# Kernel tuning notes

Hardware: AMD Instinct MI355X
Metric: run time of the kernel (lower is better)

Reference implementation:

```python
import jax, jax.numpy as jnp
import numpy as np

NUM_HEADS = 16
HEAD_DIM = 128
EMBED = NUM_HEADS * HEAD_DIM  # 2048
BATCH, SEQ = 2, 2048


def setup_inputs() -> dict:
    key = jax.random.key(0)
    k1, k2 = jax.random.split(key)
    x = jax.random.normal(k1, (BATCH, SEQ, EMBED), dtype=jnp.float32)
    W = jax.random.normal(k2, (EMBED, 3 * EMBED), dtype=jnp.float32) * 0.02
    b = jnp.zeros((3 * EMBED,), dtype=jnp.float32)
    return {"x": x, "W": W, "b": b}


def _rotate_half(u):
    u1, u2 = jnp.split(u, 2, axis=-1)
    return jnp.concatenate([-u2, u1], axis=-1)


def reference(x, W, b):
    B, S, E = x.shape
    H, D = NUM_HEADS, HEAD_DIM
    # Fused QKV projection: [B,S,E] @ [E,3E] -> [B,S,3E]
    qkv = jnp.einsum('bse,ef->bsf', x, W) + b
    qkv = qkv.reshape(B, S, 3, H, D)
    q, k, v = qkv[:, :, 0], qkv[:, :, 1], qkv[:, :, 2]  # each [B,S,H,D]
    # Module's rotary embedding: sin/cos over arange(S*D), shared across heads
    t = jnp.arange(S * D, dtype=jnp.float32).reshape(1, S, 1, D)
    sin, cos = jnp.sin(t), jnp.cos(t)
    q = q * cos + _rotate_half(q) * sin
    k = k * cos + _rotate_half(k) * sin
    # Scaled dot-product attention over sequence, per head
    scale = 1.0 / jnp.sqrt(jnp.float32(D))
    attn = jnp.einsum('bqhd,bkhd->bhqk', q, k) * scale  # [B,H,S,S]
    w = jax.nn.softmax(attn, axis=-1)
    out = jnp.einsum('bhqk,bkhd->bqhd', w, v)  # [B,S,H,D]
    return out
```

## Files before the change

### kernel.cpp

```cpp
#include <hip/hip_runtime.h>
#include <stdint.h>

typedef unsigned short u16;
typedef __attribute__((ext_vector_type(8))) short bf16x8;
typedef __attribute__((ext_vector_type(4))) float f32x4;

#define NUM_B 2
#define SEQ   2048
#define SEQP  2080
#define NH    16
#define HD    128
#define EMB   2048
#define N3    6144
#define MM    4096
#define QT    256
#define WQ    32
#define KT    64
#define NTILE (SEQ / KT)

#define BM 128
#define BN 384
#define BK 64
#define NT_K (EMB / BK)

__device__ __forceinline__ u16 f2bf(float f) {
  union { float f; unsigned u; } c; c.f = f;
  return (u16)((c.u + 0x7FFFu + ((c.u >> 16) & 1u)) >> 16);
}
__device__ __forceinline__ void async16(const void* g, void* l) {
  __builtin_amdgcn_global_load_lds(
      (const __attribute__((address_space(1))) void*)g,
      (__attribute__((address_space(3))) void*)l, 16, 0, 0);
}
__device__ __forceinline__ uint32_t cvtpk_bf16(float lo, float hi) {
  uint32_t r;
  asm("v_cvt_pk_bf16_f32 %0, %1, %2" : "=v"(r) : "v"(lo), "v"(hi));
  return r;
}

#define GBAR()   asm volatile("s_barrier" ::: "memory")

#define CVT_BLKS (MM * EMB / 4 / 256)
#define TRN_BX   (N3 / 32)
__global__ void k_prep(const float* __restrict__ x, u16* __restrict__ xb,
                       float2* __restrict__ tab,
                       const float* __restrict__ W, u16* __restrict__ Wt) {
  __shared__ float t[32][33];
  const int bid = blockIdx.x;
  if (bid < CVT_BLKS) {
    int i = bid * 256 + threadIdx.x;
    const float4 v = ((const float4*)x)[i];
    ushort4 o;
    o.x = f2bf(v.x); o.y = f2bf(v.y); o.z = f2bf(v.z); o.w = f2bf(v.w);
    ((ushort4*)xb)[i] = o;
    if (i < SEQ * HD) {
      double tt = (double)i;
      tab[i] = make_float2((float)cos(tt), (float)sin(tt));
    }
  } else {
    int b2 = bid - CVT_BLKS;
    int n0 = (b2 % TRN_BX) * 32, k0 = (b2 / TRN_BX) * 32;
    int tx = threadIdx.x & 31, ty = threadIdx.x >> 5;
    #pragma unroll
    for (int i = ty; i < 32; i += 8)
      t[i][tx] = W[(size_t)(k0 + i) * N3 + n0 + tx];
    __syncthreads();
    #pragma unroll
    for (int i = ty; i < 32; i += 8)
      Wt[(size_t)(n0 + i) * EMB + k0 + tx] = f2bf(t[tx][i]);
  }
}

__global__ __launch_bounds__(512, 2) void k_gemm_qkv(
    const u16* __restrict__ xb, const u16* __restrict__ wt,
    const float* __restrict__ bias, const float2* __restrict__ tab,
    u16* __restrict__ qb, u16* __restrict__ kb, u16* __restrict__ vbt)
{
  __shared__ __align__(16) u16 lsA[2][BM * BK];
  __shared__ __align__(16) u16 lsB[2][BN * BK];
  const int tid = threadIdx.x;
  const int wave = tid >> 6, lane = tid & 63;
  const int lq = lane & 15, lr = lane >> 4;
  const int wr = wave >> 2, wc = wave & 3;
  const int m0 = blockIdx.y * BM, n0 = blockIdx.x * BN;

  auto stA = [&](int t) {
    const int kt = t * BK;
    #pragma unroll
    for (int ii = 0; ii < 2; ++ii) {
      int s = ii * 512 + tid;
      int row = s >> 3, gq = (s & 7) ^ (row & 7);
      async16(xb + (size_t)(m0 + row) * EMB + kt + gq * 8, &lsA[t & 1][s * 8]);
    }
  };
  auto stB = [&](int t, int u) {
    const int kt = t * BK;
    #pragma unroll
    for (int ii = 0; ii < 2; ++ii) {
      int s = u * 1024 + ii * 512 + tid;
      int row = s >> 3, gq = (s & 7) ^ (row & 7);
      async16(wt + (size_t)(n0 + row) * EMB + kt + gq * 8, &lsB[t & 1][s * 8]);
    }
  };

  f32x4 acc[4][6];
  #pragma unroll
  for (int i = 0; i < 4; ++i)
    #pragma unroll
    for (int j = 0; j < 6; ++j)
      acc[i][j] = f32x4{0.f, 0.f, 0.f, 0.f};

  int rbase[6];
  #pragma unroll
  for (int nf = 0; nf < 6; ++nf) {
    int pg = 3 * wc + (nf >> 1);
    int col = (pg >> 2) * 128 + (pg & 3) * 16 + (nf & 1) * 64 + lq;
    rbase[nf] = col * BK;
  }
  const int aRow0 = (wr * 64 + lq) * BK;
  int qsw[2];
  qsw[0] = ((0 + lr) ^ (lq & 7)) * 8;
  qsw[1] = ((4 + lr) ^ (lq & 7)) * 8;

  stA(0); stB(0, 0); stB(0, 1); stB(0, 2); stB(1, 0); stB(1, 1); stB(1, 2);
  asm volatile("s_waitcnt vmcnt(6)" ::: "memory");
  GBAR();

  for (int ti = 0; ti < NT_K / 2; ++ti) {
    const int t0 = 2 * ti, t1 = t0 + 1;
    const bool nl = (ti < NT_K / 2 - 1);

    #pragma unroll
    for (int hp = 0; hp < 2; ++hp) {
      const u16* Ap = lsA[hp];
      const u16* Bp = lsB[hp];
      bf16x8 bfr[6][2];

      #pragma unroll
      for (int ph = 0; ph < 2; ++ph) {
        if (ph == 0) {
          #pragma unroll
          for (int nf = 0; nf < 6; ++nf)
            #pragma unroll
            for (int kk = 0; kk < 2; ++kk)
              bfr[nf][kk] = *(const bf16x8*)(Bp + rbase[nf] + qsw[kk]);
        }
        bf16x8 af[2][2];
        #pragma unroll
        for (int mfl = 0; mfl < 2; ++mfl)
          #pragma unroll
          for (int kk = 0; kk < 2; ++kk)
            af[mfl][kk] = *(const bf16x8*)(Ap + aRow0 + ((ph * 2 + mfl) * 16) * BK + qsw[kk]);

        if (hp == 0) {
          if (ph == 0) {
            stA(t1);
          } else {
            if (nl) {
              stB(t0 + 2, 0); stB(t0 + 2, 1);
              asm volatile("s_waitcnt vmcnt(4)" ::: "memory");
            } else {
              asm volatile("s_waitcnt vmcnt(0)" ::: "memory");
            }
          }
        } else {
          if (ph == 0) {
            if (nl) { stA(t0 + 2); stB(t0 + 2, 2); }
          } else {
            if (nl) {
              stB(t1 + 2, 0); stB(t1 + 2, 1); stB(t1 + 2, 2);
              asm volatile("s_waitcnt vmcnt(6)" ::: "memory");
            }
          }
        }

        #pragma unroll
        for (int kk = 0; kk < 2; ++kk)
          #pragma unroll
          for (int mfl = 0; mfl < 2; ++mfl)
            #pragma unroll
            for (int nf = 0; nf < 6; ++nf)
              acc[ph * 2 + mfl][nf] = __builtin_amdgcn_mfma_f32_16x16x32_bf16(
                  af[mfl][kk], bfr[nf][kk], acc[ph * 2 + mfl][nf], 0, 0, 0);
        __builtin_amdgcn_sched_barrier(0);
        GBAR();
      }
    }
  }

  const int m0w = m0 + wr * 64;
  const int bxH = n0 >> 7;
  #pragma unroll
  for (int pl = 0; pl < 3; ++pl) {
    const int pg = 3 * wc + pl;
    const int j = pg >> 2;
    const int s4 = pg & 3;
    const int H = bxH + j;
    const int w = H >> 4;
    const int h = H & 15;
    const int d1 = s4 * 16 + lq;
    const float b1 = bias[n0 + j * 128 + d1];
    const float b2 = bias[n0 + j * 128 + d1 + 64];

    if (w == 2) {
      #pragma unroll
      for (int mf = 0; mf < 4; ++mf) {
        int mg0 = m0w + mf * 16 + lr * 4;
        int b = mg0 >> 11, s0 = mg0 & 2047;
        ushort4 pk;
        pk.x = f2bf(acc[mf][2 * pl][0] + b1);
        pk.y = f2bf(acc[mf][2 * pl][1] + b1);
        pk.z = f2bf(acc[mf][2 * pl][2] + b1);
        pk.w = f2bf(acc[mf][2 * pl][3] + b1);
        *(ushort4*)(vbt + ((size_t)(b * NH + h) * HD + d1) * SEQP + s0) = pk;
        pk.x = f2bf(acc[mf][2 * pl + 1][0] + b2);
        pk.y = f2bf(acc[mf][2 * pl + 1][1] + b2);
        pk.z = f2bf(acc[mf][2 * pl + 1][2] + b2);
        pk.w = f2bf(acc[mf][2 * pl + 1][3] + b2);
        *(ushort4*)(vbt + ((size_t)(b * NH + h) * HD + d1 + 64) * SEQP + s0) = pk;
      }
    } else {
      u16* basep = (w == 0) ? qb : kb;
      const float qs = (w == 0) ? 0.12751569843736827f : 1.0f;
      #pragma unroll
      for (int mf = 0; mf < 4; ++mf)
        #pragma unroll
        for (int r = 0; r < 4; ++r) {
          int mg = m0w + mf * 16 + lr * 4 + r;
          int b = mg >> 11, s = mg & 2047;
          u16* dst = basep + ((size_t)(b * NH + h) * SEQ + s) * HD;
          float c1 = acc[mf][2 * pl][r]     + b1;
          float c2 = acc[mf][2 * pl + 1][r] + b2;
          float2 s1 = tab[s * HD + d1];
          float2 s2 = tab[s * HD + d1 + 64];
          dst[d1]      = f2bf((c1 * s1.x - c2 * s1.y) * qs);
          dst[d1 + 64] = f2bf((c2 * s2.x + c1 * s2.y) * qs);
        }
    }
  }
}

__global__ __launch_bounds__(512, 1) void k_flash(
    const u16* __restrict__ qb, const u16* __restrict__ kb,
    const u16* __restrict__ vbt, float* __restrict__ out)
{
  __shared__ __align__(16) u16 lsK[2][KT * HD];
  __shared__ __align__(16) u16 lsV[2][HD * KT];
  __shared__ __align__(16) u16 lsP[8][WQ * KT];

  const int tid = threadIdx.x;
  const int wave = tid >> 6, lane = tid & 63;
  const int lq = lane & 15, lr = lane >> 4;
  const int i = blockIdx.x;
  const int xcd = i & 7, j = i >> 3;
  const int bh = xcd * 4 + (j >> 3);
  const int q0 = (j & 7) * QT;
  const u16* Qg = qb + ((size_t)bh * SEQ + q0 + wave * WQ) * HD;
  const u16* Kg = kb + (size_t)bh * SEQ * HD;
  const u16* Vg = vbt + (size_t)bh * HD * SEQP;

  auto stage = [&](int tile, int buf) {
    const int k0 = tile * KT;
    #pragma unroll
    for (int ii = 0; ii < 2; ++ii) {
      int c = tid + ii * 512;
      int key = c >> 4, grp = c & 15;
      async16(Kg + (size_t)(k0 + key) * HD + ((grp ^ (key & 7)) * 8), lsK[buf] + c * 8);
    }
    #pragma unroll
    for (int ii = 0; ii < 2; ++ii) {
      int c = tid + ii * 512;
      int d = c >> 3, g2 = c & 7;
      async16(Vg + (size_t)d * SEQP + k0 + ((g2 ^ ((d >> 1) & 7)) * 8), lsV[buf] + c * 8);
    }
  };

  stage(0, 0);

  bf16x8 qf[2][4];
  #pragma unroll
  for (int qq = 0; qq < 2; ++qq)
    #pragma unroll
    for (int ks = 0; ks < 4; ++ks)
      qf[qq][ks] = *(const bf16x8*)(Qg + (size_t)(qq * 16 + lq) * HD + ks * 32 + lr * 8);

  f32x4 acc_o[2][8];
  float lsum[2] = {0.f, 0.f};
  #pragma unroll
  for (int mb = 0; mb < 2; ++mb)
    #pragma unroll
    for (int nb = 0; nb < 8; ++nb) acc_o[mb][nb] = f32x4{0.f, 0.f, 0.f, 0.f};

  for (int t = 0; t < NTILE; ++t) {
    const int p = t & 1;
    __syncthreads();
    if (t + 1 < NTILE) stage(t + 1, 1 - p);

    f32x4 sacc[4][2];
    #pragma unroll
    for (int kbi = 0; kbi < 4; ++kbi)
      #pragma unroll
      for (int qq = 0; qq < 2; ++qq) sacc[kbi][qq] = f32x4{0.f, 0.f, 0.f, 0.f};
    #pragma unroll
    for (int ks = 0; ks < 4; ++ks) {
      bf16x8 kf[4];
      #pragma unroll
      for (int kbi = 0; kbi < 4; ++kbi) {
        int key = kbi * 16 + lq;
        int g = (ks * 4 + lr) ^ (key & 7);
        kf[kbi] = *(const bf16x8*)(lsK[p] + key * HD + g * 8);
      }
      #pragma unroll
      for (int kbi = 0; kbi < 4; ++kbi)
        #pragma unroll
        for (int qq = 0; qq < 2; ++qq)
          sacc[kbi][qq] = __builtin_amdgcn_mfma_f32_16x16x32_bf16(kf[kbi], qf[qq][ks], sacc[kbi][qq], 0, 0, 0);
    }

    #pragma unroll
    for (int half = 0; half < 2; ++half) {
      #pragma unroll
      for (int kb2 = 0; kb2 < 2; ++kb2) {
        int kbi = half * 2 + kb2;
        #pragma unroll
        for (int qq = 0; qq < 2; ++qq) {
          float p0 = __builtin_amdgcn_exp2f(sacc[kbi][qq][0]);
          float p1 = __builtin_amdgcn_exp2f(sacc[kbi][qq][1]);
          float p2 = __builtin_amdgcn_exp2f(sacc[kbi][qq][2]);
          float p3 = __builtin_amdgcn_exp2f(sacc[kbi][qq][3]);
          lsum[qq] += (p0 + p1) + (p2 + p3);
          int row = qq * 16 + lq;
          int g = kbi * 4 + lr;
          int gp = g ^ (row & 6) ^ ((row & 8) >> 1);
          uint2 pk;
          pk.x = cvtpk_bf16(p0, p1);
          pk.y = cvtpk_bf16(p2, p3);
          *(uint2*)(lsP[wave] + row * KT + gp * 4) = pk;
        }
      }

      bf16x8 ap[2];
      #pragma unroll
      for (int mb = 0; mb < 2; ++mb) {
        int row = mb * 16 + lq;
        int sw = (row & 6) ^ ((row & 8) >> 1);
        int gb = (half * 8 + 2 * lr) ^ sw;
        ap[mb] = *(const bf16x8*)(lsP[wave] + row * KT + gb * 4);
      }
      #pragma unroll
      for (int nb = 0; nb < 8; ++nb) {
        int d = nb * 16 + lq;
        int q8 = (half * 4 + lr) ^ ((d >> 1) & 7);
        bf16x8 bv = *(const bf16x8*)(lsV[p] + d * KT + q8 * 8);
        #pragma unroll
        for (int mb = 0; mb < 2; ++mb)
          acc_o[mb][nb] = __builtin_amdgcn_mfma_f32_16x16x32_bf16(ap[mb], bv, acc_o[mb][nb], 0, 0, 0);
      }
    }
  }

  float inv[2];
  #pragma unroll
  for (int qq = 0; qq < 2; ++qq) {
    float s = lsum[qq];
    s += __shfl_xor(s, 16);
    s += __shfl_xor(s, 32);
    inv[qq] = 1.0f / s;
  }
  const int b = bh >> 4, h = bh & 15;
  #pragma unroll
  for (int mb = 0; mb < 2; ++mb)
    #pragma unroll
    for (int r = 0; r < 4; ++r) {
      float iv = __shfl(inv[mb], lr * 4 + r);
      int row = wave * WQ + mb * 16 + lr * 4 + r;
      int sq = q0 + row;
      float* op = out + (((size_t)b * SEQ + sq) * NH + h) * HD;
      #pragma unroll
      for (int nb = 0; nb < 8; ++nb)
        op[nb * 16 + lq] = acc_o[mb][nb][r] * iv;
    }
}


extern "C" void kernel_launch(void* const* d_in, const int* in_sizes, int n_in,
                              void* d_out, int out_size, void* d_ws, size_t ws_size,
                              hipStream_t stream) {
  (void)in_sizes; (void)n_in; (void)out_size; (void)ws_size;
  const float* x    = (const float*)d_in[0];
  const float* W    = (const float*)d_in[1];
  const float* bias = (const float*)d_in[2];
  float* out = (float*)d_out;

  char* p = (char*)d_ws;
  u16* xb  = (u16*)p;  p += (size_t)MM * EMB * 2;
  u16* wt  = (u16*)p;  p += (size_t)N3 * EMB * 2;
  u16* qb  = (u16*)p;  p += (size_t)NUM_B * NH * SEQ * HD * 2;
  u16* kb  = (u16*)p;  p += (size_t)NUM_B * NH * SEQ * HD * 2;
  u16* vbt = (u16*)p;  p += (size_t)NUM_B * NH * HD * SEQP * 2;
  float2* tab = (float2*)p;

  k_prep<<<CVT_BLKS + TRN_BX * (EMB / 32), 256, 0, stream>>>(x, xb, tab, W, wt);
  k_gemm_qkv<<<dim3(N3 / BN, MM / BM), 512, 0, stream>>>(xb, wt, bias, tab, qb, kb, vbt);
  k_flash<<<SEQ / QT * NUM_B * NH, 512, 0, stream>>>(qb, kb, vbt, out);
}
```

Before: 209.1 us.

## Simplify QKV GEMM pipeline to single-stage double buffer with full waits

```diff
diff --git a/kernel.cpp b/kernel.cpp
--- a/kernel.cpp
+++ b/kernel.cpp
@@ -93,11 +93,11 @@
       async16(xb + (size_t)(m0 + row) * EMB + kt + gq * 8, &lsA[t & 1][s * 8]);
     }
   };
-  auto stB = [&](int t, int u) {
+  auto stB = [&](int t) {
     const int kt = t * BK;
     #pragma unroll
-    for (int ii = 0; ii < 2; ++ii) {
-      int s = u * 1024 + ii * 512 + tid;
+    for (int ii = 0; ii < 6; ++ii) {
+      int s = ii * 512 + tid;
       int row = s >> 3, gq = (s & 7) ^ (row & 7);
       async16(wt + (size_t)(n0 + row) * EMB + kt + gq * 8, &lsB[t & 1][s * 8]);
     }
@@ -122,70 +122,41 @@
   qsw[0] = ((0 + lr) ^ (lq & 7)) * 8;
   qsw[1] = ((4 + lr) ^ (lq & 7)) * 8;
 
-  stA(0); stB(0, 0); stB(0, 1); stB(0, 2); stB(1, 0); stB(1, 1); stB(1, 2);
-  asm volatile("s_waitcnt vmcnt(6)" ::: "memory");
+  stA(0); stB(0);
+  asm volatile("s_waitcnt vmcnt(0)" ::: "memory");
   GBAR();
 
-  for (int ti = 0; ti < NT_K / 2; ++ti) {
-    const int t0 = 2 * ti, t1 = t0 + 1;
-    const bool nl = (ti < NT_K / 2 - 1);
-
-    #pragma unroll
-    for (int hp = 0; hp < 2; ++hp) {
-      const u16* Ap = lsA[hp];
-      const u16* Bp = lsB[hp];
-      bf16x8 bfr[6][2];
-
-      #pragma unroll
-      for (int ph = 0; ph < 2; ++ph) {
-        if (ph == 0) {
-          #pragma unroll
-          for (int nf = 0; nf < 6; ++nf)
-            #pragma unroll
-            for (int kk = 0; kk < 2; ++kk)
-              bfr[nf][kk] = *(const bf16x8*)(Bp + rbase[nf] + qsw[kk]);
-        }
-        bf16x8 af[2][2];
-        #pragma unroll
-        for (int mfl = 0; mfl < 2; ++mfl)
-          #pragma unroll
-          for (int kk = 0; kk < 2; ++kk)
-            af[mfl][kk] = *(const bf16x8*)(Ap + aRow0 + ((ph * 2 + mfl) * 16) * BK + qsw[kk]);
-
-        if (hp == 0) {
-          if (ph == 0) {
-            stA(t1);
-          } else {
-            if (nl) {
-              stB(t0 + 2, 0); stB(t0 + 2, 1);
-              asm volatile("s_waitcnt vmcnt(4)" ::: "memory");
-            } else {
-              asm volatile("s_waitcnt vmcnt(0)" ::: "memory");
-            }
-          }
-        } else {
-          if (ph == 0) {
-            if (nl) { stA(t0 + 2); stB(t0 + 2, 2); }
-          } else {
-            if (nl) {
-              stB(t1 + 2, 0); stB(t1 + 2, 1); stB(t1 + 2, 2);
-              asm volatile("s_waitcnt vmcnt(6)" ::: "memory");
-            }
-          }
-        }
-
-        #pragma unroll
-        for (int kk = 0; kk < 2; ++kk)
-          #pragma unroll
-          for (int mfl = 0; mfl < 2; ++mfl)
-            #pragma unroll
-            for (int nf = 0; nf < 6; ++nf)
-              acc[ph * 2 + mfl][nf] = __builtin_amdgcn_mfma_f32_16x16x32_bf16(
-                  af[mfl][kk], bfr[nf][kk], acc[ph * 2 + mfl][nf], 0, 0, 0);
-        __builtin_amdgcn_sched_barrier(0);
-        GBAR();
-      }
-    }
+  for (int t = 0; t < NT_K; ++t) {
+    const int p = t & 1;
+    const u16* Ap = lsA[p];
+    const u16* Bp = lsB[p];
+
+    bf16x8 bfr[6][2];
+    #pragma unroll
+    for (int nf = 0; nf < 6; ++nf)
+      #pragma unroll
+      for (int kk = 0; kk < 2; ++kk)
+        bfr[nf][kk] = *(const bf16x8*)(Bp + rbase[nf] + qsw[kk]);
+    bf16x8 af[4][2];
+    #pragma unroll
+    for (int mf = 0; mf < 4; ++mf)
+      #pragma unroll
+      for (int kk = 0; kk < 2; ++kk)
+        af[mf][kk] = *(const bf16x8*)(Ap + aRow0 + (mf * 16) * BK + qsw[kk]);
+
+    if (t + 1 < NT_K) { stA(t + 1); stB(t + 1); }
+
+    #pragma unroll
+    for (int kk = 0; kk < 2; ++kk)
+      #pragma unroll
+      for (int mf = 0; mf < 4; ++mf)
+        #pragma unroll
+        for (int nf = 0; nf < 6; ++nf)
+          acc[mf][nf] = __builtin_amdgcn_mfma_f32_16x16x32_bf16(
+              af[mf][kk], bfr[nf][kk], acc[mf][nf], 0, 0, 0);
+    __builtin_amdgcn_sched_barrier(0);
+    asm volatile("s_waitcnt vmcnt(0)" ::: "memory");
+    GBAR();
   }
 
   const int m0w = m0 + wr * 64;
```

Result: slower. 216.2 us (+3.4%).
